# Kernel optimization log

Hardware: AMD Instinct MI355X
Metric: run time of the kernel (lower is better)

The kernel has to match this reference:

```python
import jax, jax.numpy as jnp
import numpy as np

B, C, H, W = 2, 48, 128, 256
HEADS = 3
EPS_LN = 1e-6
EPS_NRM = 1e-12


def _conv(x, w, b, padding=0, dilation=1, groups=1):
    # x: NCHW, w: OIHW
    out = jax.lax.conv_general_dilated(
        x, w, window_strides=(1, 1),
        padding=[(padding, padding), (padding, padding)],
        rhs_dilation=(dilation, dilation),
        feature_group_count=groups,
        dimension_numbers=('NCHW', 'OIHW', 'NCHW'))
    return out + b[None, :, None, None]


def _ln2d(x, w, b):
    # LayerNorm over channel dim per pixel (NAFNet-style LayerNorm2d)
    mu = x.mean(axis=1, keepdims=True)
    var = ((x - mu) ** 2).mean(axis=1, keepdims=True)
    return (x - mu) / jnp.sqrt(var + EPS_LN) * w[None, :, None, None] + b[None, :, None, None]


def _l2norm(x):
    # F.normalize(dim=-1): x / max(||x||_2, eps)
    n = jnp.sqrt((x * x).sum(-1, keepdims=True))
    return x / jnp.maximum(n, EPS_NRM)


def setup_inputs() -> dict:
    key = jax.random.key(0)
    ks = iter(jax.random.split(key, 40))
    def nrm(shape, s=0.02):
        return jax.random.normal(next(ks), shape, jnp.float32) * s
    d = {
        'x_l': jax.random.normal(next(ks), (B, C, H, W), jnp.float32),
        'x_r': jax.random.normal(next(ks), (B, C, H, W), jnp.float32),
        'ln1_w': jnp.ones((C,), jnp.float32), 'ln1_b': jnp.zeros((C,), jnp.float32),
        'ln2_w': jnp.ones((C,), jnp.float32), 'ln2_b': jnp.zeros((C,), jnp.float32),
        'qkv_l_w': nrm((3 * C, C, 1, 1)), 'qkv_l_b': jnp.zeros((3 * C,), jnp.float32),
        'qkv_r_w': nrm((3 * C, C, 1, 1)), 'qkv_r_b': jnp.zeros((3 * C,), jnp.float32),
        'dw_l_w': nrm((3 * C, 1, 3, 3)), 'dw_l_b': jnp.zeros((3 * C,), jnp.float32),
        'dw_r_w': nrm((3 * C, 1, 3, 3)), 'dw_r_b': jnp.zeros((3 * C,), jnp.float32),
        'dil0_w': nrm((2 * C, 2 * C, 3, 3)), 'dil0_b': jnp.zeros((2 * C,), jnp.float32),
        'dil1_w': nrm((2 * C, 2 * C, 3, 3)), 'dil1_b': jnp.zeros((2 * C,), jnp.float32),
        'dil2_w': nrm((2 * C, 2 * C, 3, 3)), 'dil2_b': jnp.zeros((2 * C,), jnp.float32),
        'convQ_w': nrm((C, 6 * C, 1, 1)), 'convQ_b': jnp.zeros((C,), jnp.float32),
        'conv1_w': nrm((C, C, 1, 1)), 'conv1_b': jnp.zeros((C,), jnp.float32),
        'conv2_w': nrm((C, C, 1, 1)), 'conv2_b': jnp.zeros((C,), jnp.float32),
        'temperature': jnp.ones((HEADS, 1, 1), jnp.float32),
    }
    return d


def reference(x_l, x_r, ln1_w, ln1_b, ln2_w, ln2_b,
              qkv_l_w, qkv_l_b, qkv_r_w, qkv_r_b,
              dw_l_w, dw_l_b, dw_r_w, dw_r_b,
              dil0_w, dil0_b, dil1_w, dil1_b, dil2_w, dil2_b,
              convQ_w, convQ_b, conv1_w, conv1_b, conv2_w, conv2_b,
              temperature):
    b, c, h, w = x_l.shape
    hw = h * w
    ch = c // HEADS  # channels per head

    norm_l = _ln2d(x_l, ln1_w, ln1_b)
    norm_r = _ln2d(x_r, ln2_w, ln2_b)

    qkvl = _conv(_conv(norm_l, qkv_l_w, qkv_l_b), dw_l_w, dw_l_b, padding=1, groups=3 * c)
    qkvr = _conv(_conv(norm_r, qkv_r_w, qkv_r_b), dw_r_w, dw_r_b, padding=1, groups=3 * c)
    Q_l, K_l, V_l = jnp.split(qkvl, 3, axis=1)
    Q_r, K_r, V_r = jnp.split(qkvr, 3, axis=1)

    Q = jnp.concatenate((Q_l, Q_r), axis=1)  # [b, 2c, h, w]
    Q = jnp.concatenate((
        _conv(Q, dil0_w, dil0_b, padding=2, dilation=2),
        _conv(Q, dil1_w, dil1_b, padding=4, dilation=4),
        _conv(Q, dil2_w, dil2_b, padding=6, dilation=6)), axis=1)  # [b, 6c, h, w]
    Q = _conv(Q, convQ_w, convQ_b)  # [b, c, h, w]

    def heads(t):
        return t.reshape(b, HEADS, ch, hw)

    Q = _l2norm(heads(Q))
    K_l = _l2norm(heads(K_l))
    K_r = _l2norm(heads(K_r))
    V_l = heads(V_l)
    V_r = heads(V_r)

    # channel attention: [b, head, ch, ch]
    A_r2l = jax.nn.softmax(jnp.einsum('bhcn,bhdn->bhcd', Q, K_r) * temperature, axis=-1)
    A_l2r = jax.nn.softmax(jnp.einsum('bhcn,bhdn->bhcd', Q, K_l) * temperature, axis=-1)

    F_l = jnp.einsum('bhcd,bhdn->bhcn', A_r2l, V_l).reshape(b, c, h, w)
    F_r = jnp.einsum('bhcd,bhdn->bhcn', A_l2r, V_r).reshape(b, c, h, w)

    F_l = _conv(F_l, conv1_w, conv1_b)
    F_r = _conv(F_r, conv2_w, conv2_b)
    return (x_l + F_l, x_r + F_r)
```

## Files before the change

### kernel.cpp

```cpp
#include <hip/hip_runtime.h>
#include <hip/hip_bf16.h>

typedef __hip_bfloat16 bf16;
typedef __attribute__((ext_vector_type(8))) short short8;
typedef __attribute__((ext_vector_type(4))) float f32x4;
typedef unsigned int u32;

constexpr int IMG_H = 128;
constexpr int IMG_W = 256;
constexpr int HW    = IMG_H * IMG_W;
constexpr int BB    = 2;
constexpr int CC    = 48;
constexpr int C3    = 144;
constexpr int XPW   = 268;
constexpr int XOFF  = 6;
constexpr int QCP   = 104;
constexpr int QCS   = XPW * QCP;
constexpr int QCH   = QCS / 2;

constexpr int WO_QKVL_W = 0;
constexpr int WO_QKVR_W = 6912;
constexpr int WO_DWL_W  = 13824;
constexpr int WO_DWR_W  = 15120;
constexpr int WO_C1_W   = 16416;
constexpr int WO_C2_W   = 18720;
constexpr int WO_QKVL_B = 21024;
constexpr int WO_QKVR_B = 21168;
constexpr int WO_DWL_B  = 21312;
constexpr int WO_DWR_B  = 21456;
constexpr int WO_C1_B   = 21600;
constexpr int WO_C2_B   = 21648;
constexpr int WO_LN1W   = 21696;
constexpr int WO_LN1B   = 21744;
constexpr int WO_LN2W   = 21792;
constexpr int WO_LN2B   = 21840;
constexpr int WO_TEMP   = 21888;
constexpr int WO_WQ     = 21952;
constexpr int WO_D0W    = 35776;
constexpr int WO_BQ     = 284608;
constexpr int WO_B0     = 284656;
constexpr int WO_B1     = 284752;
constexpr int WO_B2     = 284848;
constexpr int WO_WPACK  = 284944;
constexpr int WO_EFFB   = 409360;
constexpr int WO_AR2L   = 409712;
constexpr int WO_AL2R   = 411248;
constexpr int WO_M1     = 412800;
constexpr int WO_M2     = 417408;
constexpr int WO_WQP    = 422016;
constexpr int WO_PART   = 431232;
constexpr int WO_PART2  = WO_D0W;

constexpr size_t ACT_BASE_BYTES = 2118144;

constexpr size_t A_P  = 0;
constexpr size_t A_Q1 = 9437184;
constexpr size_t A_Q2 = 18874368;
constexpr size_t A_QC = 28311552;

constexpr int NPREP = 22;
struct PrepArgs {
  const void* src[NPREP];
  int dst[NPREP];
  int n[NPREP];
  int cstart[NPREP];
};

__device__ __forceinline__ bool probe_bf16(const void* ln1w) {
  return ((const unsigned short*)ln1w)[0] == 0x3F80;
}

__global__ __launch_bounds__(256) void prep_k(PrepArgs a, float* __restrict__ wsf) {
  bool isb = probe_bf16(a.src[12]);
  int chunk = blockIdx.x;
  int t = 0;
#pragma unroll 1
  while (t < NPREP - 1 && chunk >= a.cstart[t + 1]) ++t;
  int i = (chunk - a.cstart[t]) * 256 + threadIdx.x;
  if (i < a.n[t]) {
    float v = isb ? __bfloat162float(((const bf16*)a.src[t])[i])
                  : ((const float*)a.src[t])[i];
    wsf[a.dst[t] + i] = v;
  }
}

__global__ __launch_bounds__(512) void effw2_k(
    const float* __restrict__ wsf, const void* __restrict__ dwa,
    const void* __restrict__ dwb, const void* __restrict__ dwc,
    const void* __restrict__ probe, bf16* __restrict__ wpack) {
  int d  = blockIdx.x / 96;
  int ci = blockIdx.x % 96;
  __shared__ float wds[864];
  __shared__ float wqs[48 * 97];
  const void* dwp = (d == 0) ? dwa : (d == 1) ? dwb : dwc;
  bool isb = probe_bf16(probe);
  for (int idx = threadIdx.x; idx < 864; idx += 512) {
    int m = idx / 9, tt = idx % 9;
    int e = (m * 96 + ci) * 9 + tt;
    wds[idx] = isb ? __bfloat162float(((const bf16*)dwp)[e])
                   : ((const float*)dwp)[e];
  }
  for (int idx = threadIdx.x; idx < 4608; idx += 512) {
    int co = idx / 96, m = idx % 96;
    wqs[co * 97 + m] = wsf[WO_WQ + co * 288 + d * 96 + m];
  }
  __syncthreads();
  int tco = threadIdx.x;
  if (tco < 432) {
    int t = tco / 48, co = tco % 48;
    float s = 0.f;
#pragma unroll 8
    for (int m = 0; m < 96; ++m) s += wqs[co * 97 + m] * wds[m * 9 + t];
    int trow = t / 3, dxi = t % 3;
    int ti = (trow == 0) ? (2 - d) * 3 + dxi
           : (trow == 1) ? 9 + d * 3 + dxi
                         : 18 + d * 3 + dxi;
    int kc = ci >> 5, j = ci & 7;
    int L = ((ci & 31) >> 3) * 16 + (co & 15);
    int nt = co >> 4;
    int f = (ti * 3 + kc) * 3 + nt;
    wpack[(size_t)f * 512 + L * 8 + j] = __float2bfloat16(s);
  }
}

__global__ __launch_bounds__(256) void wqp_k(const float* __restrict__ wsf,
                                             bf16* __restrict__ wqp,
                                             float* __restrict__ effb) {
  if (blockIdx.x == 72) {
    int co = threadIdx.x;
    if (co < 48) {
      float s = wsf[WO_BQ + co];
      for (int m = 0; m < 96; ++m) {
        s += wsf[WO_WQ + co * 288 + m]       * wsf[WO_B0 + m];
        s += wsf[WO_WQ + co * 288 + 96 + m]  * wsf[WO_B1 + m];
        s += wsf[WO_WQ + co * 288 + 192 + m] * wsf[WO_B2 + m];
      }
      effb[co] = s;
    }
    return;
  }
  int idx = blockIdx.x * 256 + threadIdx.x;
  if (idx >= 18432) return;
  int side = idx / 9216;
  int rem = idx % 9216;
  int nt = rem / 1024;
  int kt = (rem / 512) % 2;
  int e  = rem % 512;
  int L = e >> 3, j = e & 7;
  int o = nt * 16 + (L & 15);
  int kp = kt * 32 + (L >> 4) * 8 + j;
  int g = kp >> 4, r = kp & 15;
  float val = 0.f;
  if (r < 12) {
    int c = g * 12 + r;
    val = wsf[(side ? WO_QKVR_W : WO_QKVL_W) + o * 48 + c];
  }
  wqp[idx] = __float2bfloat16(val);
}

__global__ __launch_bounds__(256) void lnqkv_k(
    const void* __restrict__ x, const void* __restrict__ probe,
    const float* __restrict__ lnw, const float* __restrict__ lnb,
    const bf16* __restrict__ wqp_side, const float* __restrict__ qb,
    bf16* __restrict__ pre) {
  __shared__ __align__(16) unsigned char LDSU[21504 + 18432];
  bf16* XNs = (bf16*)LDSU;
  float2* red = (float2*)(LDSU + 9216);
  bf16* Cs = (bf16*)LDSU;
  bf16* W = (bf16*)(LDSU + 21504);
  int tid = threadIdx.x;
  for (int i = tid; i < 1152; i += 256)
    ((uint4*)W)[i] = ((const uint4*)wqp_side)[i];

  int px = tid & 63;
  int w = tid >> 6;
  int p = blockIdx.x * 64 + px;
  int b = p >> 15;
  int pix = p & (HW - 1);
  size_t base = (size_t)b * CC * HW + pix;
  float v[12];
  if (probe_bf16(probe)) {
    const bf16* xp = (const bf16*)x + base;
#pragma unroll
    for (int c = 0; c < 12; ++c)
      v[c] = __bfloat162float(xp[(size_t)(w * 12 + c) * HW]);
  } else {
    const float* xp = (const float*)x + base;
#pragma unroll
    for (int c = 0; c < 12; ++c) v[c] = xp[(size_t)(w * 12 + c) * HW];
  }
  float s = 0.f, s2 = 0.f;
#pragma unroll
  for (int c = 0; c < 12; ++c) { s += v[c]; s2 += v[c] * v[c]; }
  red[w * 64 + px] = make_float2(s, s2);
  __syncthreads();
  float S = 0.f, S2 = 0.f;
#pragma unroll
  for (int i = 0; i < 4; ++i) {
    float2 r2 = red[i * 64 + px];
    S += r2.x; S2 += r2.y;
  }
  float mu = S * (1.f / 48.f);
  float var = S2 * (1.f / 48.f) - mu * mu;
  float rs = rsqrtf(var + 1e-6f);
  bf16 o16[16];
#pragma unroll
  for (int c = 0; c < 12; ++c)
    o16[c] = __float2bfloat16((v[c] - mu) * rs * lnw[w * 12 + c] + lnb[w * 12 + c]);
#pragma unroll
  for (int c = 12; c < 16; ++c) o16[c] = __float2bfloat16(0.f);
  *(uint4*)(XNs + px * 72 + w * 16) = *(uint4*)(o16);
  *(uint4*)(XNs + px * 72 + w * 16 + 8) = *(uint4*)(o16 + 8);
  __syncthreads();

  int L = tid & 63;
  int lo = L & 15, hi = L >> 4;
  const bf16* arow = XNs + (size_t)(w * 16 + lo) * 72 + hi * 8;
  short8 a0 = *(const short8*)(arow);
  short8 a1 = *(const short8*)(arow + 32);
  __syncthreads();
#pragma unroll
  for (int nt = 0; nt < 9; ++nt) {
    float bvv = qb[nt * 16 + lo];
    f32x4 acc = {bvv, bvv, bvv, bvv};
    acc = __builtin_amdgcn_mfma_f32_16x16x32_bf16(
        a0, *(const short8*)(W + (nt * 2 + 0) * 512 + L * 8), acc, 0, 0, 0);
    acc = __builtin_amdgcn_mfma_f32_16x16x32_bf16(
        a1, *(const short8*)(W + (nt * 2 + 1) * 512 + L * 8), acc, 0, 0, 0);
#pragma unroll
    for (int r = 0; r < 4; ++r)
      Cs[(nt * 16 + lo) * 66 + w * 16 + hi * 4 + r] = __float2bfloat16(acc[r]);
  }
  __syncthreads();
  int pix0 = (blockIdx.x * 64) & (HW - 1);
#pragma unroll
  for (int pass = 0; pass < 18; ++pass) {
    int o = pass * 8 + (tid >> 5);
    int px2 = (tid & 31) * 2;
    bf16 t2[2];
    t2[0] = Cs[o * 66 + px2];
    t2[1] = Cs[o * 66 + px2 + 1];
    *(unsigned*)(pre + ((size_t)(b * C3 + o)) * HW + pix0 + px2) = *(unsigned*)t2;
  }
}

__global__ __launch_bounds__(256) void dw_k(
    const bf16* __restrict__ in, const float* __restrict__ w9,
    const float* __restrict__ bias, bf16* __restrict__ out) {
  int gid = blockIdx.x;
  int yt = gid & 15;
  int c = (gid >> 4) % C3;
  int b = gid / (16 * C3);
  int ry = threadIdx.x >> 5, xi = threadIdx.x & 31;
  int y = yt * 8 + ry;
  int x0 = xi * 8;
  const bf16* base = in + ((size_t)(b * C3 + c)) * HW;
  float wv[9];
#pragma unroll
  for (int t = 0; t < 9; ++t) wv[t] = w9[c * 9 + t];
  float bz = bias[c];
  float acc[8];
#pragma unroll
  for (int i = 0; i < 8; ++i) acc[i] = bz;
#pragma unroll
  for (int ky = 0; ky < 3; ++ky) {
    int yy = y + ky - 1;
    if ((unsigned)yy >= (unsigned)IMG_H) continue;
    const bf16* row = base + yy * IMG_W + x0;
    uint4 m = *(const uint4*)(row);
    float f[10];
    f[0] = (x0 > 0) ? __bfloat162float(row[-1]) : 0.f;
    f[9] = (x0 + 8 < IMG_W) ? __bfloat162float(row[8]) : 0.f;
    f[1] = __uint_as_float(m.x << 16);
    f[2] = __uint_as_float(m.x & 0xFFFF0000u);
    f[3] = __uint_as_float(m.y << 16);
    f[4] = __uint_as_float(m.y & 0xFFFF0000u);
    f[5] = __uint_as_float(m.z << 16);
    f[6] = __uint_as_float(m.z & 0xFFFF0000u);
    f[7] = __uint_as_float(m.w << 16);
    f[8] = __uint_as_float(m.w & 0xFFFF0000u);
    float w0 = wv[ky * 3], w1 = wv[ky * 3 + 1], w2 = wv[ky * 3 + 2];
#pragma unroll
    for (int i = 0; i < 8; ++i)
      acc[i] += w0 * f[i] + w1 * f[i + 1] + w2 * f[i + 2];
  }
  bf16 o[8];
#pragma unroll
  for (int i = 0; i < 8; ++i) o[i] = __float2bfloat16(acc[i]);
  *(uint4*)(out + ((size_t)(b * C3 + c)) * HW + y * IMG_W + x0) = *(uint4*)o;
}

__global__ __launch_bounds__(256) void qc_k(const bf16* __restrict__ q1,
                                            const bf16* __restrict__ q2,
                                            bf16* __restrict__ qc) {
  int b = blockIdx.x >> 7;
  int y = blockIdx.x & 127;
  int half = blockIdx.y;
  int tid = threadIdx.x;
  int x0 = half * 128;
  int px = tid & 127;
  int cig = tid >> 7;
  __shared__ __align__(16) bf16 T[128][100];
#pragma unroll 8
  for (int k = 0; k < 48; ++k) {
    int ci = cig * 48 + k;
    const bf16* src = (ci < 48)
        ? q1 + (((size_t)(b * C3 + ci)) * IMG_H + y) * IMG_W
        : q2 + (((size_t)(b * C3 + ci - 48)) * IMG_H + y) * IMG_W;
    T[px][ci] = src[x0 + px];
  }
  __syncthreads();
  size_t rowbase = ((size_t)(b * IMG_H + y)) * QCS;
#pragma unroll 1
  for (int i = 0; i < 14; ++i) {
    int e4 = i * 256 + tid;
    if (e4 >= QCH / 4) break;
    int e = e4 * 4 + half * QCH;
    int xp = e / QCP;
    int cin = e % QCP;
    int x = xp - XOFF;
    uint2 val;
    val.x = 0u; val.y = 0u;
    if ((unsigned)x < (unsigned)IMG_W && cin < 96) {
      val = *(const uint2*)(&T[x - x0][cin]);
    }
    *(uint2*)(qc + rowbase + e) = val;
  }
}

__global__ __launch_bounds__(256, 2) void dil_mfma_k(
    const bf16* __restrict__ qc, const bf16* __restrict__ wp,
    const float* __restrict__ effb, bf16* __restrict__ qh) {
  __shared__ __align__(16) unsigned char LDSU[29120];
  bf16* Arow = (bf16*)LDSU;
  float* Cs  = (float*)LDSU;
  constexpr int WCH = 140 * QCP / 8;

  int bid = blockIdx.x;
  int xcd = bid & 7;
  int rest = bid >> 3;
  int y = xcd * 16 + (rest & 15);
  int half = (rest >> 4) & 1;
  int b = rest >> 5;
  int x0 = half * 128;
  int tid = threadIdx.x;
  int L = tid & 63;
  int w = tid >> 6;
  int lo = L & 15, hi = L >> 4;

  f32x4 acc[2][3];
#pragma unroll
  for (int g2 = 0; g2 < 2; ++g2)
#pragma unroll
    for (int nt = 0; nt < 3; ++nt) {
      float bv = effb[nt * 16 + lo];
      acc[g2][nt] = {bv, bv, bv, bv};
    }

  const bf16* wrow = wp + L * 8;
  short8 wc[9];
#pragma unroll
  for (int f = 0; f < 9; ++f)
    wc[f] = *(const short8*)(wrow + f * 512);

  int dy_prev = -100;
#pragma unroll 1
  for (int g = 0; g < 9; ++g) {
    int D = (g < 3) ? (6 - 2 * g) : (g < 6) ? (2 * (g - 2)) : (2 * (g - 5));
    int dy = (g < 3) ? -D : (g < 6) ? 0 : D;
    int yy = y + dy;
    bool valid = (unsigned)yy < (unsigned)IMG_H;
    if (valid && dy != dy_prev) {
      __syncthreads();
      const bf16* src = qc + (size_t)(b * IMG_H + yy) * QCS + (size_t)x0 * QCP;
#pragma unroll
      for (int r = 0; r < 8; ++r) {
        int c = w + r * 4;
        int i = c * 64 + L;
        if (i < WCH) {
          __builtin_amdgcn_global_load_lds(
              (const __attribute__((address_space(1))) u32*)(src + (size_t)i * 8),
              (__attribute__((address_space(3))) u32*)(Arow + (size_t)c * 512),
              16, 0, 0);
        }
      }
      __syncthreads();
      dy_prev = dy;
    }
#pragma unroll
    for (int dxi = 0; dxi < 3; ++dxi) {
      int ti = g * 3 + dxi;
      short8 wn[9];
      if (ti < 26) {
        const bf16* wr = wrow + (ti + 1) * 4608;
#pragma unroll
        for (int f = 0; f < 9; ++f)
          wn[f] = *(const short8*)(wr + f * 512);
      }
      if (valid) {
        int dx = (dxi - 1) * D;
        const bf16* ar = Arow + (size_t)(XOFF + dx + w * 32 + lo) * QCP + hi * 8;
#pragma unroll
        for (int g2 = 0; g2 < 2; ++g2)
#pragma unroll
          for (int kc = 0; kc < 3; ++kc) {
            short8 a = *(const short8*)(ar + g2 * (16 * QCP) + kc * 32);
#pragma unroll
            for (int nt = 0; nt < 3; ++nt)
              acc[g2][nt] = __builtin_amdgcn_mfma_f32_16x16x32_bf16(
                  a, wc[kc * 3 + nt], acc[g2][nt], 0, 0, 0);
          }
      }
      if (ti < 26) {
#pragma unroll
        for (int f = 0; f < 9; ++f) wc[f] = wn[f];
      }
    }
  }

  __syncthreads();
#pragma unroll
  for (int g2 = 0; g2 < 2; ++g2)
#pragma unroll
    for (int nt = 0; nt < 3; ++nt)
#pragma unroll
      for (int r = 0; r < 4; ++r)
        Cs[(nt * 16 + lo) * 132 + w * 32 + g2 * 16 + hi * 4 + r] = acc[g2][nt][r];
  __syncthreads();
  size_t obase = (size_t)b * CC * HW + (size_t)y * IMG_W + x0;
#pragma unroll
  for (int i = 0; i < 6; ++i) {
    int chunk = i * 256 + tid;
    int co = chunk >> 5;
    int px4 = (chunk & 31) * 4;
    const float* s = Cs + co * 132 + px4;
    bf16 t4[4];
    t4[0] = __float2bfloat16(s[0]);
    t4[1] = __float2bfloat16(s[1]);
    t4[2] = __float2bfloat16(s[2]);
    t4[3] = __float2bfloat16(s[3]);
    *(uint2*)(qh + obase + (size_t)co * HW + px4) = *(uint2*)t4;
  }
}

__device__ __forceinline__ float blo(unsigned u) {
  return __uint_as_float(u << 16);
}
__device__ __forceinline__ float bhi(unsigned u) {
  return __uint_as_float(u & 0xFFFF0000u);
}

__global__ __launch_bounds__(256) void logits_mfma_k(
    const bf16* __restrict__ qh, const bf16* __restrict__ qkvl,
    const bf16* __restrict__ qkvr, float* __restrict__ part,
    float* __restrict__ part2) {
  int abh = blockIdx.x;
  int chunk = blockIdx.y;
  int a = abh / 6;
  int b = (abh / 3) % 2;
  int h = abh % 3;
  int tid = threadIdx.x;
  int L = tid & 63, w = tid >> 6;
  int lo = L & 15, hi = L >> 4;
  const bf16* qrow = qh + ((size_t)(b * CC + h * 16 + lo)) * HW;
  const bf16* krow =
      ((a == 0) ? qkvr : qkvl) + ((size_t)(b * C3 + 48 + h * 16 + lo)) * HW;
  int px0 = chunk * 1024 + w * 256 + hi * 8;
  f32x4 acc = {0.f, 0.f, 0.f, 0.f};
  float aq = 0.f, ak = 0.f;
#pragma unroll
  for (int s = 0; s < 8; ++s) {
    short8 av = *(const short8*)(qrow + px0 + s * 32);
    short8 bv = *(const short8*)(krow + px0 + s * 32);
    acc = __builtin_amdgcn_mfma_f32_16x16x32_bf16(av, bv, acc, 0, 0, 0);
#pragma unroll
    for (int j = 0; j < 4; ++j) {
      u32 ua = ((const u32*)&av)[j];
      u32 ub = ((const u32*)&bv)[j];
      float q0 = blo(ua), q1 = bhi(ua);
      float k0 = blo(ub), k1 = bhi(ub);
      aq += q0 * q0 + q1 * q1;
      ak += k0 * k0 + k1 * k1;
    }
  }
  __shared__ float red[4][256];
  __shared__ float sq[256], sk[256];
#pragma unroll
  for (int r = 0; r < 4; ++r) red[w][(hi * 4 + r) * 16 + lo] = acc[r];
  sq[tid] = aq;
  sk[tid] = ak;
  __syncthreads();
  float sum = red[0][tid] + red[1][tid] + red[2][tid] + red[3][tid];
  part[((size_t)abh * 32 + chunk) * 256 + tid] = sum;
  if (tid < 32) {
    const float* srcr = (tid < 16) ? sq : sk;
    int lo2 = tid & 15;
    float s = 0.f;
#pragma unroll
    for (int w2 = 0; w2 < 4; ++w2)
#pragma unroll
      for (int h2 = 0; h2 < 4; ++h2) s += srcr[w2 * 64 + h2 * 16 + lo2];
    part2[((size_t)abh * 32 + chunk) * 32 + tid] = s;
  }
}

__global__ __launch_bounds__(256) void logits_red_k(
    const float* __restrict__ part, const float* __restrict__ part2,
    const float* __restrict__ temp, float* __restrict__ logr2l,
    float* __restrict__ logl2r) {
  int abh = blockIdx.x;
  int a = abh / 6, h = abh % 3;
  int bnum = (abh / 3) % 2;
  int t = threadIdx.x;
  int i = t >> 4, j = t & 15;
  __shared__ float nrm[32];
  if (t < 32) {
    float s = 0.f;
    const float* p2 = part2 + (size_t)abh * 32 * 32 + t;
#pragma unroll 8
    for (int c = 0; c < 32; ++c) s += p2[c * 32];
    nrm[t] = fmaxf(sqrtf(s), 1e-12f);
  }
  float s = 0.f;
  const float* p = part + (size_t)abh * 32 * 256 + t;
#pragma unroll 8
  for (int c = 0; c < 32; ++c) s += p[c * 256];
  __syncthreads();
  float val = s / (nrm[i] * nrm[16 + j]) * temp[h];
  ((a == 0) ? logr2l : logl2r)[bnum * 768 + h * 256 + i * 16 + j] = val;
}

__global__ __launch_bounds__(256) void softmaxM_k(float* __restrict__ wsf) {
  int tid = threadIdx.x;
  __shared__ float A1[1536], A2[1536];
  if (tid < 192) {
    const float* p = wsf + ((tid < 96) ? WO_AR2L : WO_AL2R) + (tid % 96) * 16;
    float* dst = ((tid < 96) ? A1 : A2) + (tid % 96) * 16;
    float m = -1e30f;
#pragma unroll
    for (int j = 0; j < 16; ++j) m = fmaxf(m, p[j]);
    float s = 0.f;
    float e[16];
#pragma unroll
    for (int j = 0; j < 16; ++j) {
      e[j] = expf(p[j] - m);
      s += e[j];
    }
    float inv = 1.f / s;
#pragma unroll
    for (int j = 0; j < 16; ++j) dst[j] = e[j] * inv;
  }
  __syncthreads();
#pragma unroll 1
  for (int idx = tid; idx < 4608; idx += 256) {
    int b = idx / 2304;
    int r = idx % 2304;
    int o = r / 48;
    int cp = r % 48;
    int h = cp >> 4, j = cp & 15;
    const float* a1 = &A1[((b * 3 + h) * 16) * 16 + j];
    const float* a2 = &A2[((b * 3 + h) * 16) * 16 + j];
    float s1 = 0.f, s2 = 0.f;
#pragma unroll
    for (int i = 0; i < 16; ++i) {
      s1 += wsf[WO_C1_W + o * 48 + h * 16 + i] * a1[i * 16];
      s2 += wsf[WO_C2_W + o * 48 + h * 16 + i] * a2[i * 16];
    }
    wsf[WO_M1 + idx] = s1;
    wsf[WO_M2 + idx] = s2;
  }
}

__global__ __launch_bounds__(256) void attn_out2_k(
    const bf16* __restrict__ q1, const bf16* __restrict__ q2,
    const void* __restrict__ x1, const void* __restrict__ x2,
    const void* __restrict__ probe, const float* __restrict__ Mall,
    const float* __restrict__ cball, void* __restrict__ out) {
  int side = blockIdx.y;
  const bf16* qkv = side ? q2 : q1;
  const void* x = side ? x2 : x1;
  const float* M = Mall + side * 4608;
  const float* cb = cball + side * 48;
  int tid = threadIdx.x;
  int p = blockIdx.x * 256 + tid;
  int b = __builtin_amdgcn_readfirstlane(p >> 15);
  int pix = p & (HW - 1);
  bool isb = probe_bf16(probe);

  float v[CC];
  const bf16* vb = qkv + ((size_t)(b * C3 + 96)) * HW + pix;
#pragma unroll
  for (int c = 0; c < CC; ++c) v[c] = __bfloat162float(vb[(size_t)c * HW]);

  const float* Mb = M + b * 2304;
  size_t base = (size_t)b * CC * HW + pix;
  size_t obase = (size_t)side * BB * CC * HW + base;
  if (isb) {
    const bf16* xp = (const bf16*)x + base;
    bf16* op = (bf16*)out + obase;
#pragma unroll 4
    for (int o = 0; o < CC; ++o) {
      float acc = cb[o];
      const float* mrow = Mb + o * 48;
#pragma unroll
      for (int c = 0; c < CC; ++c) acc += mrow[c] * v[c];
      op[(size_t)o * HW] =
          __float2bfloat16(acc + __bfloat162float(xp[(size_t)o * HW]));
    }
  } else {
    const float* xp = (const float*)x + base;
    float* op = (float*)out + obase;
#pragma unroll 4
    for (int o = 0; o < CC; ++o) {
      float acc = cb[o];
      const float* mrow = Mb + o * 48;
#pragma unroll
      for (int c = 0; c < CC; ++c) acc += mrow[c] * v[c];
      op[(size_t)o * HW] = acc + xp[(size_t)o * HW];
    }
  }
}

extern "C" void kernel_launch(void* const* d_in, const int* in_sizes, int n_in,
                              void* d_out, int out_size, void* d_ws, size_t ws_size,
                              hipStream_t stream) {
  (void)in_sizes; (void)n_in; (void)out_size; (void)ws_size;
  const void* x_l = d_in[0];
  const void* x_r = d_in[1];
  const void* probe = d_in[2];
  float* wsf = (float*)d_ws;
  bf16* wpack = (bf16*)(wsf + WO_WPACK);
  bf16* wqp = (bf16*)(wsf + WO_WQP);
  bf16* act = (bf16*)((char*)d_ws + ACT_BASE_BYTES);
  bf16* P  = act + A_P;
  bf16* Q1 = act + A_Q1;
  bf16* Q2 = act + A_Q2;
  bf16* QC = act + A_QC;
  bf16* qh = P;

  PrepArgs pa;
  const int srcIdx[NPREP] = {6, 8, 10, 12, 22, 24, 7, 9, 11, 13, 23, 25,
                             2, 3, 4, 5, 26, 20, 21, 15, 17, 19};
  const int dstOff[NPREP] = {WO_QKVL_W, WO_QKVR_W, WO_DWL_W, WO_DWR_W, WO_C1_W,
                             WO_C2_W, WO_QKVL_B, WO_QKVR_B, WO_DWL_B, WO_DWR_B,
                             WO_C1_B, WO_C2_B, WO_LN1W, WO_LN1B, WO_LN2W,
                             WO_LN2B, WO_TEMP, WO_WQ, WO_BQ, WO_B0, WO_B1, WO_B2};
  const int ns[NPREP] = {6912, 6912, 1296, 1296, 2304, 2304, 144, 144, 144, 144,
                         48, 48, 48, 48, 48, 48, 3, 13824, 48, 96, 96, 96};
  int ck = 0;
  for (int i = 0; i < NPREP; ++i) {
    pa.src[i] = d_in[srcIdx[i]];
    pa.dst[i] = dstOff[i];
    pa.n[i] = ns[i];
    pa.cstart[i] = ck;
    ck += (ns[i] + 255) / 256;
  }
  prep_k<<<ck, 256, 0, stream>>>(pa, wsf);

  effw2_k<<<288, 512, 0, stream>>>(wsf, d_in[14], d_in[16], d_in[18],
                                   probe, wpack);
  wqp_k<<<73, 256, 0, stream>>>(wsf, wqp, wsf + WO_EFFB);

  lnqkv_k<<<1024, 256, 0, stream>>>(x_l, probe, wsf + WO_LN1W, wsf + WO_LN1B,
                                    wqp, wsf + WO_QKVL_B, P);
  dw_k<<<BB * C3 * 16, 256, 0, stream>>>(P, wsf + WO_DWL_W, wsf + WO_DWL_B, Q1);
  lnqkv_k<<<1024, 256, 0, stream>>>(x_r, probe, wsf + WO_LN2W, wsf + WO_LN2B,
                                    wqp + 9216, wsf + WO_QKVR_B, P);
  dw_k<<<BB * C3 * 16, 256, 0, stream>>>(P, wsf + WO_DWR_W, wsf + WO_DWR_B, Q2);

  qc_k<<<dim3(BB * IMG_H, 2), 256, 0, stream>>>(Q1, Q2, QC);

  dil_mfma_k<<<512, 256, 0, stream>>>(QC, wpack, wsf + WO_EFFB, qh);

  logits_mfma_k<<<dim3(12, 32), 256, 0, stream>>>(qh, Q1, Q2, wsf + WO_PART,
                                                  wsf + WO_PART2);
  logits_red_k<<<12, 256, 0, stream>>>(wsf + WO_PART, wsf + WO_PART2,
                                       wsf + WO_TEMP, wsf + WO_AR2L,
                                       wsf + WO_AL2R);
  softmaxM_k<<<1, 256, 0, stream>>>(wsf);

  attn_out2_k<<<dim3(256, 2), 256, 0, stream>>>(
      Q1, Q2, x_l, x_r, probe, wsf + WO_M1, wsf + WO_C1_B, d_out);
}
```

Before: 277.6 us.

## Process full image rows per block and stage dilated-conv weights through LDS

The dilated-conv MFMA kernel now runs 512-thread blocks, each covering a full 256-pixel row instead of half a row, so the padded input row is loaded into LDS once per block rather than twice. Per-tap weights are no longer held in registers and reloaded from global by every wave. They are double-buffered in LDS with async global_load_lds, and a barrier follows each tap. This cuts redundant global traffic for weights and halo overlap and frees registers. In exchange it adds 27 block-wide syncs, more LDS per block (about 74KB, which limits occupancy), and half as many blocks.

```diff
diff --git a/kernel.cpp b/kernel.cpp
--- a/kernel.cpp
+++ b/kernel.cpp
@@ -17,6 +17,7 @@
 constexpr int QCP   = 104;
 constexpr int QCS   = XPW * QCP;
 constexpr int QCH   = QCS / 2;
+constexpr int QCCH  = QCS / 8;
 
 constexpr int WO_QKVL_W = 0;
 constexpr int WO_QKVR_W = 6912;
@@ -328,21 +329,19 @@
   }
 }
 
-__global__ __launch_bounds__(256, 2) void dil_mfma_k(
+__global__ __launch_bounds__(512, 2) void dil_mfma_k(
     const bf16* __restrict__ qc, const bf16* __restrict__ wp,
     const float* __restrict__ effb, bf16* __restrict__ qh) {
-  __shared__ __align__(16) unsigned char LDSU[29120];
+  __shared__ __align__(16) unsigned char LDSU[55744 + 18432];
   bf16* Arow = (bf16*)LDSU;
+  bf16* Wb   = (bf16*)(LDSU + 55744);
   float* Cs  = (float*)LDSU;
-  constexpr int WCH = 140 * QCP / 8;
 
   int bid = blockIdx.x;
   int xcd = bid & 7;
   int rest = bid >> 3;
   int y = xcd * 16 + (rest & 15);
-  int half = (rest >> 4) & 1;
-  int b = rest >> 5;
-  int x0 = half * 128;
+  int b = rest >> 4;
   int tid = threadIdx.x;
   int L = tid & 63;
   int w = tid >> 6;
@@ -357,11 +356,16 @@
       acc[g2][nt] = {bv, bv, bv, bv};
     }
 
-  const bf16* wrow = wp + L * 8;
-  short8 wc[9];
-#pragma unroll
-  for (int f = 0; f < 9; ++f)
-    wc[f] = *(const short8*)(wrow + f * 512);
+#pragma unroll
+  for (int k = 0; k < 2; ++k) {
+    int c = w + k * 8;
+    if (c < 9) {
+      __builtin_amdgcn_global_load_lds(
+          (const __attribute__((address_space(1))) u32*)(wp + c * 512 + L * 8),
+          (__attribute__((address_space(3))) u32*)(Wb + c * 512 + L * 8),
+          16, 0, 0);
+    }
+  }
 
   int dy_prev = -100;
 #pragma unroll 1
@@ -372,12 +376,12 @@
     bool valid = (unsigned)yy < (unsigned)IMG_H;
     if (valid && dy != dy_prev) {
       __syncthreads();
-      const bf16* src = qc + (size_t)(b * IMG_H + yy) * QCS + (size_t)x0 * QCP;
-#pragma unroll
-      for (int r = 0; r < 8; ++r) {
-        int c = w + r * 4;
+      const bf16* src = qc + (size_t)(b * IMG_H + yy) * QCS;
+#pragma unroll
+      for (int r = 0; r < 7; ++r) {
+        int c = w + r * 8;
         int i = c * 64 + L;
-        if (i < WCH) {
+        if (i < QCCH) {
           __builtin_amdgcn_global_load_lds(
               (const __attribute__((address_space(1))) u32*)(src + (size_t)i * 8),
               (__attribute__((address_space(3))) u32*)(Arow + (size_t)c * 512),
@@ -390,14 +394,22 @@
 #pragma unroll
     for (int dxi = 0; dxi < 3; ++dxi) {
       int ti = g * 3 + dxi;
-      short8 wn[9];
       if (ti < 26) {
-        const bf16* wr = wrow + (ti + 1) * 4608;
-#pragma unroll
-        for (int f = 0; f < 9; ++f)
-          wn[f] = *(const short8*)(wr + f * 512);
+        const bf16* srcw = wp + (ti + 1) * 4608;
+        bf16* dstw = Wb + ((ti + 1) & 1) * 4608;
+#pragma unroll
+        for (int k = 0; k < 2; ++k) {
+          int c = w + k * 8;
+          if (c < 9) {
+            __builtin_amdgcn_global_load_lds(
+                (const __attribute__((address_space(1))) u32*)(srcw + c * 512 + L * 8),
+                (__attribute__((address_space(3))) u32*)(dstw + c * 512 + L * 8),
+                16, 0, 0);
+          }
+        }
       }
       if (valid) {
+        const bf16* wb = Wb + (ti & 1) * 4608;
         int dx = (dxi - 1) * D;
         const bf16* ar = Arow + (size_t)(XOFF + dx + w * 32 + lo) * QCP + hi * 8;
 #pragma unroll
@@ -408,32 +420,29 @@
 #pragma unroll
             for (int nt = 0; nt < 3; ++nt)
               acc[g2][nt] = __builtin_amdgcn_mfma_f32_16x16x32_bf16(
-                  a, wc[kc * 3 + nt], acc[g2][nt], 0, 0, 0);
+                  a, *(const short8*)(wb + (kc * 3 + nt) * 512 + L * 8),
+                  acc[g2][nt], 0, 0, 0);
           }
       }
-      if (ti < 26) {
-#pragma unroll
-        for (int f = 0; f < 9; ++f) wc[f] = wn[f];
-      }
-    }
-  }
-
-  __syncthreads();
+      __syncthreads();
+    }
+  }
+
 #pragma unroll
   for (int g2 = 0; g2 < 2; ++g2)
 #pragma unroll
     for (int nt = 0; nt < 3; ++nt)
 #pragma unroll
       for (int r = 0; r < 4; ++r)
-        Cs[(nt * 16 + lo) * 132 + w * 32 + g2 * 16 + hi * 4 + r] = acc[g2][nt][r];
-  __syncthreads();
-  size_t obase = (size_t)b * CC * HW + (size_t)y * IMG_W + x0;
+        Cs[(nt * 16 + lo) * 260 + w * 32 + g2 * 16 + hi * 4 + r] = acc[g2][nt][r];
+  __syncthreads();
+  size_t obase = (size_t)b * CC * HW + (size_t)y * IMG_W;
 #pragma unroll
   for (int i = 0; i < 6; ++i) {
-    int chunk = i * 256 + tid;
-    int co = chunk >> 5;
-    int px4 = (chunk & 31) * 4;
-    const float* s = Cs + co * 132 + px4;
+    int chunk = i * 512 + tid;
+    int co = chunk >> 6;
+    int px4 = (chunk & 63) * 4;
+    const float* s = Cs + co * 260 + px4;
     bf16 t4[4];
     t4[0] = __float2bfloat16(s[0]);
     t4[1] = __float2bfloat16(s[1]);
@@ -670,7 +679,7 @@
 
   qc_k<<<dim3(BB * IMG_H, 2), 256, 0, stream>>>(Q1, Q2, QC);
 
-  dil_mfma_k<<<512, 256, 0, stream>>>(QC, wpack, wsf + WO_EFFB, qh);
+  dil_mfma_k<<<256, 512, 0, stream>>>(QC, wpack, wsf + WO_EFFB, qh);
 
   logits_mfma_k<<<dim3(12, 32), 256, 0, stream>>>(qh, Q1, Q2, wsf + WO_PART,
                                                   wsf + WO_PART2);
```

New measurement: 278.1 us. No clear change (+0.2%).
